# Optimization experiments

Hardware: AMD Instinct MI355X
Metric: run time of the kernel (lower is better)

The kernel has to match this reference:

```python
import jax, jax.numpy as jnp
import numpy as np

BSZ, IN_DIM, OUT_DIM = 512, 1024, 2048
M_AND = 5        # Anderson memory (self.m)
BETA = 1.0
LAM = 1e-4
ALPHA = 1.0
TOL = 1e-5
MAX_ITER = 50
M_MON = 1.0      # monotonicity parameter of MONSingleFc


def _multiply(A, B, z):
    # MONSingleFc.multiply: (1-m)z - z A^T A + z B^T - z B
    Az = z @ A.T
    return (1.0 - M_MON) * z - Az @ A + z @ B.T - z @ B


def _relu(z):
    return jnp.maximum(z, 0.0)


def _single_it(A, B, z, bias):
    zn = _multiply(A, B, z)
    zn = (1.0 - ALPHA) * z + ALPHA * (zn + bias)
    zn = _relu(zn)
    err = jnp.linalg.norm(zn - z) / (1e-6 + jnp.linalg.norm(zn))
    return zn, err


def _anderson_solve(A, B, bias):
    bsz, d = bias.shape
    dt = bias.dtype
    Z = jnp.zeros((bsz, M_AND, d), dt)
    F = jnp.zeros((bsz, M_AND, d), dt)
    z0 = jnp.zeros((bsz, d), dt)
    f0, _ = _single_it(A, B, z0, bias)
    F = F.at[:, 0].set(f0)
    Z = Z.at[:, 1].set(f0)
    f1, _ = _single_it(A, B, f0, bias)
    F = F.at[:, 1].set(f1)
    eye = jnp.eye(M_AND, dtype=dt)

    def cond(s):
        Z, F, it, err = s
        return (it < MAX_ITER) & (err > TOL)

    def body(s):
        Z, F, it, _ = s
        n = jnp.minimum(M_AND, it)
        mask = jnp.arange(M_AND) < n                         # active Anderson slots
        # For it < m the unused slots of Z and F are still zero, so G = F - Z
        # has zero rows there and GGt's Frobenius norm matches the :n slice.
        G = F - Z                                            # (bsz, m, d)
        GGt = jnp.einsum('bmd,bnd->bmn', G, G)
        nrm = jnp.linalg.norm(GGt.reshape(GGt.shape[0], -1), axis=-1)
        GGt = GGt / (nrm[:, None, None] + 1e-6)
        pair = mask[:, None] & mask[None, :]
        # identity padding on inactive slots keeps the solve well-posed and
        # yields alpha = 0 there, equivalent to slicing [:n+1, :n+1].
        Hb = jnp.where(pair, GGt + LAM * eye, eye)
        mk = mask.astype(dt)
        H = jnp.zeros((bsz, M_AND + 1, M_AND + 1), dt)
        H = H.at[:, 0, 1:].set(mk).at[:, 1:, 0].set(mk).at[:, 1:, 1:].set(Hb)
        y = jnp.zeros((bsz, M_AND + 1, 1), dt).at[:, 0, 0].set(1.0)
        alpha = jnp.linalg.solve(H, y)[:, 1:, 0]             # (bsz, m)
        z_new = BETA * jnp.einsum('bm,bmd->bd', alpha, F) \
              + (1.0 - BETA) * jnp.einsum('bm,bmd->bd', alpha, Z)
        slot = it % M_AND
        Z = Z.at[:, slot].set(z_new)
        zo, err = _single_it(A, B, z_new, bias)
        F = F.at[:, slot].set(zo)
        return Z, F, it + 1, err

    Z, F, it, err = jax.lax.while_loop(
        cond, body, (Z, F, jnp.array(2, jnp.int32), jnp.array(jnp.inf, dt)))
    slot = (it - 1) % M_AND
    return Z[:, slot]


def setup_inputs():
    key = jax.random.key(0)
    kx, ka, kb, kw, kub = jax.random.split(key, 5)
    s = 1.0 / np.sqrt(OUT_DIM).astype(np.float32)
    x = jax.random.normal(kx, (BSZ, IN_DIM), jnp.float32)
    # scaled so ||W|| < 1 -> forward-backward splitting converges (trained MON regime)
    A = 0.3 * s * jax.random.normal(ka, (OUT_DIM, OUT_DIM), jnp.float32)
    B = 0.1 * s * jax.random.normal(kb, (OUT_DIM, OUT_DIM), jnp.float32)
    U_W = (1.0 / np.sqrt(IN_DIM).astype(np.float32)) * jax.random.normal(kw, (OUT_DIM, IN_DIM), jnp.float32)
    U_b = 0.01 * jax.random.normal(kub, (OUT_DIM,), jnp.float32)
    return {"x": x, "A": A, "B": B, "U_W": U_W, "U_b": U_b}


def reference(x, A, B, U_W, U_b):
    bias = x @ U_W.T + U_b                       # linear_module.bias(x)
    z_star = _anderson_solve(A, B, bias)         # equilibrium (no-grad in torch)
    zn = _relu(_multiply(A, B, z_star) + bias)   # final full step: nonlin(linear(x, z*))
    return zn
```

## Files before the change

### kernel.cpp

```cpp
#include <hip/hip_runtime.h>
#include <hip/hip_bf16.h>
#include <math.h>

#define BSZ      512
#define IN_DIM   1024
#define OUT_DIM  2048
#define M_AND    5
#define LAM      1e-4f
#define TOL      1e-5f
#define MAX_ITER 50
#define SPLIT_IT 24
#define NBLK     256
#define ITERBLK  512

typedef __bf16 bf16x8 __attribute__((ext_vector_type(8)));
typedef float  f32x4  __attribute__((ext_vector_type(4)));
typedef unsigned short u16x8 __attribute__((ext_vector_type(8)));
typedef unsigned short u16x4 __attribute__((ext_vector_type(4)));
typedef __hip_bfloat16 bf16;

#define GAS __attribute__((address_space(1)))
#define LAS __attribute__((address_space(3)))

#define S_WAITCNT_VMCNT(N) asm volatile("s_waitcnt vmcnt(" #N ")" ::: "memory")

union BU { bf16 b; unsigned short u; };

__device__ __forceinline__ float bf2f(unsigned short u) {
    union { unsigned int i; float f; } c; c.i = (unsigned int)u << 16; return c.f;
}
__device__ __forceinline__ unsigned short f2bf(float f) {
    BU t; t.b = __float2bfloat16(f); return t.u;
}

static constexpr size_t BIAS_B = 0;
static constexpr size_t F_B    = BIAS_B + (size_t)BSZ * OUT_DIM * 4;
static constexpr size_t G_B    = F_B    + (size_t)BSZ * M_AND * OUT_DIM * 4;
static constexpr size_t ZH_B   = G_B    + (size_t)BSZ * M_AND * OUT_DIM * 2;
static constexpr size_t ZL_B   = ZH_B   + (size_t)BSZ * OUT_DIM * 2;
static constexpr size_t XH_B   = ZL_B   + (size_t)BSZ * OUT_DIM * 2;
static constexpr size_t XL_B   = XH_B   + (size_t)BSZ * IN_DIM * 2;
static constexpr size_t UH_B   = XL_B   + (size_t)BSZ * IN_DIM * 2;
static constexpr size_t UL_B   = UH_B   + (size_t)OUT_DIM * IN_DIM * 2;
static constexpr size_t AT_B   = UL_B   + (size_t)OUT_DIM * IN_DIM * 2;
static constexpr size_t WT_B   = AT_B   + (size_t)OUT_DIM * OUT_DIM * 2;
static constexpr size_t RED_B  = WT_B   + (size_t)OUT_DIM * OUT_DIM * 2;
static constexpr size_t BAR_B  = RED_B  + 512;
static constexpr size_t CTR_B  = BAR_B  + 64;
static constexpr size_t FLAG_B = CTR_B  + 256;
static constexpr size_t FSLOT_B = FLAG_B + 16;
static constexpr size_t CTRL_SZ = 512 + 64 + 256 + 16 + 16;

template<int ROUNDS>
__device__ __forceinline__ void stage_tile(const void* __restrict__ g0, int row_bytes,
                                           void* l0, int tid)
{
    #pragma unroll
    for (int q = 0; q < ROUNDS; ++q) {
        const int D   = q * 4096 + tid * 16;
        const int r   = D >> 7;
        const int cb  = D & 127;
        const int scb = cb ^ ((r & 7) << 4);
        const char* gsrc = (const char*)g0 + (size_t)r * row_bytes + scb;
        char* ldst = (char*)l0 + q * 4096 + (tid >> 6) * 1024;
        __builtin_amdgcn_global_load_lds((const GAS void*)gsrc, (LAS void*)ldst, 16, 0, 0);
    }
}

__device__ __forceinline__ bf16x8 read_frag(const void* tile, int row, int cb)
{
    return *(const bf16x8*)((const char*)tile + row * 128 + (cb ^ ((row & 7) << 4)));
}

__device__ __forceinline__ void gsync(unsigned int* bar)
{
    __syncthreads();
    if (threadIdx.x == 0) {
        __threadfence();
        const unsigned int g =
            __hip_atomic_load(&bar[1], __ATOMIC_ACQUIRE, __HIP_MEMORY_SCOPE_AGENT);
        const unsigned int a =
            __hip_atomic_fetch_add(&bar[0], 1u, __ATOMIC_ACQ_REL, __HIP_MEMORY_SCOPE_AGENT);
        if (a == NBLK - 1) {
            __hip_atomic_store(&bar[0], 0u, __ATOMIC_RELAXED, __HIP_MEMORY_SCOPE_AGENT);
            __hip_atomic_fetch_add(&bar[1], 1u, __ATOMIC_RELEASE, __HIP_MEMORY_SCOPE_AGENT);
        } else {
            while (__hip_atomic_load(&bar[1], __ATOMIC_ACQUIRE, __HIP_MEMORY_SCOPE_AGENT) == g)
                __builtin_amdgcn_s_sleep(1);
        }
        __threadfence();
    }
    __syncthreads();
}

__global__ __launch_bounds__(256)
void conv_hilo(const float* __restrict__ src, bf16* __restrict__ h, bf16* __restrict__ l)
{
    const size_t i4 = ((size_t)blockIdx.x * 256 + threadIdx.x) * 4;
    const float4 v = *(const float4*)&src[i4];
    const float vv[4] = {v.x, v.y, v.z, v.w};
    union { short4 s4; unsigned short u[4]; } ph, pl;
    #pragma unroll
    for (int j = 0; j < 4; ++j) {
        ph.u[j] = f2bf(vv[j]);
        pl.u[j] = f2bf(vv[j] - bf2f(ph.u[j]));
    }
    *(short4*)((char*)h + i4 * 2) = ph.s4;
    *(short4*)((char*)l + i4 * 2) = pl.s4;
}

__global__ __launch_bounds__(256)
void prep_at(const float* __restrict__ A, bf16* __restrict__ At)
{
    __shared__ float t[64][65];
    const int tid = threadIdx.x;
    const int k0 = blockIdx.y * 64, c0 = blockIdx.x * 64;
    const int cc = tid & 63, rr = tid >> 6;
    #pragma unroll
    for (int q = 0; q < 16; ++q)
        t[rr + 4 * q][cc] = A[(size_t)(k0 + rr + 4 * q) * OUT_DIM + c0 + cc];
    __syncthreads();
    #pragma unroll
    for (int q = 0; q < 16; ++q)
        At[(size_t)(c0 + rr + 4 * q) * OUT_DIM + k0 + cc] = __float2bfloat16(t[cc][rr + 4 * q]);
}

__global__ __launch_bounds__(256)
void w_mfma(const bf16* __restrict__ At, const float* __restrict__ Bm, bf16* __restrict__ Wt)
{
    __shared__ __align__(16) bf16 lds[2][2][64 * 64];
    const int tid = threadIdx.x;
    const int lane = tid & 63, wid = tid >> 6;
    const int wy = wid >> 1, wx = wid & 1;

    int bb = blockIdx.x;
    int ti = (int)((sqrtf(8.f * bb + 1.f) - 1.f) * 0.5f);
    while ((ti + 1) * (ti + 2) / 2 <= bb) ++ti;
    while (ti * (ti + 1) / 2 > bb) --ti;
    const int tj = bb - ti * (ti + 1) / 2;
    const int r0 = ti * 64, c0 = tj * 64;
    const bool diag = (ti == tj);

    f32x4 acc[2][2];
    #pragma unroll
    for (int i = 0; i < 2; ++i)
        #pragma unroll
        for (int j = 0; j < 2; ++j) acc[i][j] = 0;

    stage_tile<2>(At + (size_t)r0 * OUT_DIM, OUT_DIM * 2, lds[0][0], tid);
    stage_tile<2>(At + (size_t)c0 * OUT_DIM, OUT_DIM * 2, lds[0][1], tid);
    __syncthreads();
    int cur = 0;
    for (int t = 0; t < 32; ++t) {
        if (t + 1 < 32) {
            const int kk = (t + 1) * 64;
            stage_tile<2>(At + (size_t)r0 * OUT_DIM + kk, OUT_DIM * 2, lds[cur ^ 1][0], tid);
            stage_tile<2>(At + (size_t)c0 * OUT_DIM + kk, OUT_DIM * 2, lds[cur ^ 1][1], tid);
        }
        const bf16* Ta = lds[cur][0];
        const bf16* Tb = lds[cur][1];
        #pragma unroll
        for (int kf = 0; kf < 2; ++kf) {
            const int cb = kf * 64 + (lane >> 4) * 16;
            bf16x8 bfr[2];
            #pragma unroll
            for (int nj = 0; nj < 2; ++nj)
                bfr[nj] = read_frag(Tb, wx * 32 + nj * 16 + (lane & 15), cb);
            #pragma unroll
            for (int mi = 0; mi < 2; ++mi) {
                bf16x8 afr = read_frag(Ta, wy * 32 + mi * 16 + (lane & 15), cb);
                #pragma unroll
                for (int nj = 0; nj < 2; ++nj)
                    acc[mi][nj] = __builtin_amdgcn_mfma_f32_16x16x32_bf16(afr, bfr[nj], acc[mi][nj], 0, 0, 0);
            }
        }
        __syncthreads();
        cur ^= 1;
    }

    #pragma unroll
    for (int mi = 0; mi < 2; ++mi) {
        const int rb = r0 + wy * 32 + mi * 16 + (lane >> 4) * 4;
        #pragma unroll
        for (int nj = 0; nj < 2; ++nj) {
            const int c = c0 + wx * 32 + nj * 16 + (lane & 15);
            const float4 bc = *(const float4*)&Bm[(size_t)c * OUT_DIM + rb];
            const float bcv[4] = {bc.x, bc.y, bc.z, bc.w};
            union { short4 s4; unsigned short u[4]; } p;
            #pragma unroll
            for (int g = 0; g < 4; ++g) {
                const float a = acc[mi][nj][g];
                const float brc = Bm[(size_t)(rb + g) * OUT_DIM + c];
                const float w = bcv[g] - brc - a;
                p.u[g] = f2bf(w);
                if (!diag) {
                    const float wm = brc - bcv[g] - a;
                    *((unsigned short*)Wt + (size_t)(rb + g) * OUT_DIM + c) = f2bf(wm);
                }
            }
            *(short4*)((char*)Wt + ((size_t)c * OUT_DIM + rb) * 2) = p.s4;
        }
    }
}

__global__ __launch_bounds__(256)
void bias_mfma(const bf16* __restrict__ xh, const bf16* __restrict__ xl,
               const bf16* __restrict__ uh, const bf16* __restrict__ ul,
               const float* __restrict__ Ub, float* __restrict__ bias,
               float* __restrict__ F, unsigned short* __restrict__ G,
               unsigned short* __restrict__ zh, unsigned short* __restrict__ zl)
{
    __shared__ __align__(16) bf16 lds[2][4][64 * 64];
    const int tid = threadIdx.x;
    const int lane = tid & 63, wid = tid >> 6;
    const int wy = wid >> 1, wx = wid & 1;
    const int m0 = blockIdx.y * 64, n0 = blockIdx.x * 64;

    f32x4 acc[2][2];
    #pragma unroll
    for (int i = 0; i < 2; ++i)
        #pragma unroll
        for (int j = 0; j < 2; ++j) acc[i][j] = 0;

    stage_tile<2>(xh + (size_t)m0 * IN_DIM, IN_DIM * 2, lds[0][0], tid);
    stage_tile<2>(xl + (size_t)m0 * IN_DIM, IN_DIM * 2, lds[0][1], tid);
    stage_tile<2>(uh + (size_t)n0 * IN_DIM, IN_DIM * 2, lds[0][2], tid);
    stage_tile<2>(ul + (size_t)n0 * IN_DIM, IN_DIM * 2, lds[0][3], tid);
    __syncthreads();
    int cur = 0;
    for (int t = 0; t < 16; ++t) {
        if (t + 1 < 16) {
            const int kk = (t + 1) * 64;
            stage_tile<2>(xh + (size_t)m0 * IN_DIM + kk, IN_DIM * 2, lds[cur ^ 1][0], tid);
            stage_tile<2>(xl + (size_t)m0 * IN_DIM + kk, IN_DIM * 2, lds[cur ^ 1][1], tid);
            stage_tile<2>(uh + (size_t)n0 * IN_DIM + kk, IN_DIM * 2, lds[cur ^ 1][2], tid);
            stage_tile<2>(ul + (size_t)n0 * IN_DIM + kk, IN_DIM * 2, lds[cur ^ 1][3], tid);
        }
        const bf16* Txh = lds[cur][0];
        const bf16* Txl = lds[cur][1];
        const bf16* Tuh = lds[cur][2];
        const bf16* Tul = lds[cur][3];
        #pragma unroll
        for (int kf = 0; kf < 2; ++kf) {
            const int cb = kf * 64 + (lane >> 4) * 16;
            bf16x8 bh[2], bl[2];
            #pragma unroll
            for (int nj = 0; nj < 2; ++nj) {
                const int br = wx * 32 + nj * 16 + (lane & 15);
                bh[nj] = read_frag(Tuh, br, cb);
                bl[nj] = read_frag(Tul, br, cb);
            }
            #pragma unroll
            for (int mi = 0; mi < 2; ++mi) {
                const int ar = wy * 32 + mi * 16 + (lane & 15);
                bf16x8 ah = read_frag(Txh, ar, cb);
                bf16x8 al = read_frag(Txl, ar, cb);
                #pragma unroll
                for (int nj = 0; nj < 2; ++nj) {
                    acc[mi][nj] = __builtin_amdgcn_mfma_f32_16x16x32_bf16(ah, bh[nj], acc[mi][nj], 0, 0, 0);
                    acc[mi][nj] = __builtin_amdgcn_mfma_f32_16x16x32_bf16(ah, bl[nj], acc[mi][nj], 0, 0, 0);
                    acc[mi][nj] = __builtin_amdgcn_mfma_f32_16x16x32_bf16(al, bh[nj], acc[mi][nj], 0, 0, 0);
                }
            }
        }
        __syncthreads();
        cur ^= 1;
    }

    #pragma unroll
    for (int mi = 0; mi < 2; ++mi) {
        const int mb = m0 + wy * 32 + mi * 16 + (lane >> 4) * 4;
        #pragma unroll
        for (int nj = 0; nj < 2; ++nj) {
            const int n = n0 + wx * 32 + nj * 16 + (lane & 15);
            const float ub = Ub[n];
            #pragma unroll
            for (int g = 0; g < 4; ++g) {
                const int m = mb + g;
                const size_t idx = (size_t)m * OUT_DIM + n;
                const float v = acc[mi][nj][g] + ub;
                bias[idx] = v;
                const float f = fmaxf(v, 0.f);
                F[((size_t)m * M_AND + 0) * OUT_DIM + n] = f;
                G[((size_t)m * M_AND + 0) * OUT_DIM + n] = f2bf(f);
                const unsigned short h = f2bf(f);
                zh[idx] = h;
                zl[idx] = f2bf(f - bf2f(h));
            }
        }
    }
}

template<bool DO_ERR>
__device__ __forceinline__ void iter_core(
    const int m0, const int n0, const int tid,
    const unsigned short* __restrict__ zh, const unsigned short* __restrict__ zl,
    const bf16* __restrict__ Wt, const float* __restrict__ bias,
    float* __restrict__ F, unsigned short* __restrict__ G,
    float* red, bf16* lds_buf, const int slot, const int it)
{
    const int lane = tid & 63, wid = tid >> 6;
    const int wy = wid >> 1, wx = wid & 1;
    #define BUFP(s) (lds_buf + (s) * 8192)

    f32x4 acc[2];
    acc[0] = 0; acc[1] = 0;

    auto STAGE = [&](int s, int kk) {
        stage_tile<1>(zh + (size_t)m0 * OUT_DIM + kk, OUT_DIM * 2, BUFP(s), tid);
        stage_tile<1>(zl + (size_t)m0 * OUT_DIM + kk, OUT_DIM * 2, BUFP(s) + 2048, tid);
        stage_tile<2>(Wt + (size_t)n0 * OUT_DIM + kk, OUT_DIM * 2, BUFP(s) + 4096, tid);
    };

    STAGE(0, 0);
    STAGE(1, 64);
    for (int t = 0; t < 32; ++t) {
        const int s = t % 3;
        if (t + 2 < 32) { S_WAITCNT_VMCNT(4); } else { S_WAITCNT_VMCNT(0); }
        __builtin_amdgcn_s_barrier();
        if (t + 2 < 32) STAGE((t + 2) % 3, (t + 2) * 64);
        const bf16* Th = BUFP(s);
        const bf16* Tl = BUFP(s) + 2048;
        const bf16* Tw = BUFP(s) + 4096;
        __builtin_amdgcn_s_setprio(1);
        #pragma unroll
        for (int kf = 0; kf < 2; ++kf) {
            const int cb = kf * 64 + (lane >> 4) * 16;
            bf16x8 b0 = read_frag(Tw, wx * 32 + (lane & 15), cb);
            bf16x8 b1 = read_frag(Tw, wx * 32 + 16 + (lane & 15), cb);
            bf16x8 ah = read_frag(Th, wy * 16 + (lane & 15), cb);
            bf16x8 al = read_frag(Tl, wy * 16 + (lane & 15), cb);
            acc[0] = __builtin_amdgcn_mfma_f32_16x16x32_bf16(ah, b0, acc[0], 0, 0, 0);
            acc[0] = __builtin_amdgcn_mfma_f32_16x16x32_bf16(al, b0, acc[0], 0, 0, 0);
            acc[1] = __builtin_amdgcn_mfma_f32_16x16x32_bf16(ah, b1, acc[1], 0, 0, 0);
            acc[1] = __builtin_amdgcn_mfma_f32_16x16x32_bf16(al, b1, acc[1], 0, 0, 0);
        }
        __builtin_amdgcn_s_setprio(0);
    }
    #undef BUFP

    float lnum = 0.f, lden = 0.f;
    const int mb = m0 + wy * 16 + (lane >> 4) * 4;
    #pragma unroll
    for (int nj = 0; nj < 2; ++nj) {
        const int n = n0 + wx * 32 + nj * 16 + (lane & 15);
        #pragma unroll
        for (int g = 0; g < 4; ++g) {
            const int m = mb + g;
            const size_t idx = (size_t)m * OUT_DIM + n;
            float v = acc[nj][g] + bias[idx];
            v = fmaxf(v, 0.f);
            const float zc = bf2f(zh[idx]) + bf2f(zl[idx]);
            const float gg = v - zc;
            F[((size_t)m * M_AND + slot) * OUT_DIM + n] = v;
            G[((size_t)m * M_AND + slot) * OUT_DIM + n] = f2bf(gg);
            if (DO_ERR) { lnum += gg * gg; lden += v * v; }
        }
    }

    if (DO_ERR) {
        #pragma unroll
        for (int off = 32; off; off >>= 1) {
            lnum += __shfl_down(lnum, off);
            lden += __shfl_down(lden, off);
        }
        __shared__ float swn[4], swd[4];
        if ((tid & 63) == 0) { swn[tid >> 6] = lnum; swd[tid >> 6] = lden; }
        __syncthreads();
        if (tid == 0) {
            atomicAdd(&red[2 * it],     swn[0] + swn[1] + swn[2] + swn[3]);
            atomicAdd(&red[2 * it + 1], swd[0] + swd[1] + swd[2] + swd[3]);
        }
    }
}

__device__ __forceinline__ void swz_mn(int bid, int& m0, int& n0)
{
    const int xcd = bid & 7, sl = bid >> 3;
    n0 = (xcd * 4 + (sl & 3)) * 64;
    m0 = (sl >> 2) * 32;
}

template<bool DO_ERR>
__global__ __launch_bounds__(256)
void iter_mfma(const unsigned short* __restrict__ zh, const unsigned short* __restrict__ zl,
               const bf16* __restrict__ Wt, const float* __restrict__ bias,
               float* __restrict__ F, unsigned short* __restrict__ G,
               float* red, unsigned int* ctr, int* flag, int* fslot, int slot, int it)
{
    if (((volatile int*)flag)[0]) return;
    __shared__ __align__(16) bf16 lds_buf[3 * 8192];
    int m0, n0;
    swz_mn(blockIdx.x, m0, n0);
    iter_core<DO_ERR>(m0, n0, threadIdx.x, zh, zl, Wt, bias, F, G, red, lds_buf, slot, it);
    if (DO_ERR && threadIdx.x == 0) {
        __threadfence();
        const unsigned int done = atomicAdd(&ctr[it], 1u);
        if (done == ITERBLK - 1) {
            ((volatile int*)fslot)[0] = slot;
            const float num2 = ((volatile float*)red)[2 * it];
            const float den2 = ((volatile float*)red)[2 * it + 1];
            if (sqrtf(num2) <= TOL * (1e-6f + sqrtf(den2)))
                ((volatile int*)flag)[0] = 1;
        }
    }
}

__global__ __launch_bounds__(256)
void final_copy(const float* __restrict__ F, const int* __restrict__ fslot,
                float* __restrict__ out)
{
    const int s = ((volatile const int*)fslot)[0];
    const size_t i4 = ((size_t)blockIdx.x * 256 + threadIdx.x) * 4;
    const int m = (int)(i4 >> 11), n = (int)(i4 & 2047);
    *(float4*)&out[i4] = *(const float4*)&F[((size_t)m * M_AND + s) * OUT_DIM + n];
}

__global__ __launch_bounds__(512)
void anderson_kernel(const float* __restrict__ F, const unsigned short* __restrict__ G,
                     unsigned short* __restrict__ zh, unsigned short* __restrict__ zl,
                     int* flag, int it)
{
    if (((volatile int*)flag)[0]) return;
    const int b = blockIdx.x;
    const int tid = threadIdx.x;
    const int lane = tid & 63, wid = tid >> 6;
    const int n = (it < M_AND) ? it : M_AND;
    const int c0 = tid * 4;
    const unsigned short* Gb = G + (size_t)b * M_AND * OUT_DIM;
    const float* Fb = F + (size_t)b * M_AND * OUT_DIM;

    float g[M_AND][4];
    float4 f[M_AND];
    #pragma unroll
    for (int m = 0; m < M_AND; ++m) {
        f[m] = *(const float4*)(Fb + (size_t)m * OUT_DIM + c0);
        if (m < n) {
            const u16x4 gv = *(const u16x4*)(Gb + (size_t)m * OUT_DIM + c0);
            #pragma unroll
            for (int q = 0; q < 4; ++q) g[m][q] = bf2f(gv[q]);
        } else {
            #pragma unroll
            for (int q = 0; q < 4; ++q) g[m][q] = 0.f;
        }
    }

    float dots[15];
    {
        int p = 0;
        #pragma unroll
        for (int i = 0; i < M_AND; ++i)
            #pragma unroll
            for (int j = i; j < M_AND; ++j) {
                float s = 0.f;
                #pragma unroll
                for (int q = 0; q < 4; ++q) s += g[i][q] * g[j][q];
                dots[p++] = s;
            }
    }

    __shared__ float sred[15][8];
    #pragma unroll
    for (int p = 0; p < 15; ++p) {
        float v = dots[p];
        #pragma unroll
        for (int off = 32; off; off >>= 1) v += __shfl_xor(v, off);
        if (lane == 0) sred[p][wid] = v;
    }
    __syncthreads();

    __shared__ float s_alpha[M_AND];
    if (tid == 0) {
        float GGm[M_AND][M_AND];
        int p = 0;
        for (int i = 0; i < M_AND; ++i)
            for (int j = i; j < M_AND; ++j) {
                float v = 0.f;
                for (int w = 0; w < 8; ++w) v += sred[p][w];
                GGm[i][j] = v; GGm[j][i] = v; ++p;
            }
        float fro = 0.f;
        for (int i = 0; i < M_AND; ++i)
            for (int j = 0; j < M_AND; ++j) fro += GGm[i][j] * GGm[i][j];
        const float inv = 1.f / (sqrtf(fro) + 1e-6f);

        float Mm[M_AND][M_AND];
        for (int i = 0; i < n; ++i)
            for (int j = 0; j < n; ++j)
                Mm[i][j] = GGm[i][j] * inv + (i == j ? LAM : 0.f);

        float L[M_AND][M_AND];
        for (int i = 0; i < n; ++i)
            for (int j = 0; j <= i; ++j) {
                float s = Mm[i][j];
                for (int k = 0; k < j; ++k) s -= L[i][k] * L[j][k];
                L[i][j] = (i == j) ? sqrtf(fmaxf(s, 1e-20f)) : s / L[j][j];
            }
        float y[M_AND], u[M_AND];
        for (int i = 0; i < n; ++i) {
            float s = 1.f;
            for (int k = 0; k < i; ++k) s -= L[i][k] * y[k];
            y[i] = s / L[i][i];
        }
        for (int i = n - 1; i >= 0; --i) {
            float s = y[i];
            for (int k = i + 1; k < n; ++k) s -= L[k][i] * u[k];
            u[i] = s / L[i][i];
        }
        float su = 0.f;
        for (int i = 0; i < n; ++i) su += u[i];
        const float isu = 1.f / su;
        for (int m = 0; m < M_AND; ++m) s_alpha[m] = (m < n) ? u[m] * isu : 0.f;
    }
    __syncthreads();

    float z[4] = {};
    #pragma unroll
    for (int m = 0; m < M_AND; ++m) {
        if (m < n) {
            const float a = s_alpha[m];
            z[0] += a * f[m].x; z[1] += a * f[m].y;
            z[2] += a * f[m].z; z[3] += a * f[m].w;
        }
    }
    u16x4 hv, lv;
    #pragma unroll
    for (int q = 0; q < 4; ++q) {
        const unsigned short h = f2bf(z[q]);
        hv[q] = h;
        lv[q] = f2bf(z[q] - bf2f(h));
    }
    *(u16x4*)(zh + (size_t)b * OUT_DIM + c0) = hv;
    *(u16x4*)(zl + (size_t)b * OUT_DIM + c0) = lv;
}

__global__ __launch_bounds__(256)
void tail_loop(unsigned short* zh, unsigned short* zl,
               const bf16* __restrict__ Wt, const float* __restrict__ bias,
               float* F, unsigned short* G,
               float* red, unsigned int* bar, int* flag, int* fslot)
{
    if (((volatile int*)flag)[0]) return;
    __shared__ __align__(16) bf16 lds_buf[3 * 8192];
    __shared__ float sred2[2][2][15];
    __shared__ float s_alpha[2][M_AND];
    const int bid = blockIdx.x, tid = threadIdx.x;
    int m0a, n0a, m0b, n0b;
    swz_mn(bid, m0a, n0a);
    swz_mn(bid + 256, m0b, n0b);

    for (int it = SPLIT_IT; it < MAX_ITER; ++it) {
        {
            const int half = tid >> 7, lt = tid & 127;
            const int r = bid * 2 + half;
            const int wv = lt >> 6;
            const unsigned short* Gb = G + (size_t)r * M_AND * OUT_DIM;
            const float* Fb = F + (size_t)r * M_AND * OUT_DIM;
            const int c0 = lt * 16;

            float g[M_AND][16];
            #pragma unroll
            for (int m = 0; m < M_AND; ++m) {
                const u16x8 ga = *(const u16x8*)(Gb + (size_t)m * OUT_DIM + c0);
                const u16x8 gb2 = *(const u16x8*)(Gb + (size_t)m * OUT_DIM + c0 + 8);
                #pragma unroll
                for (int q = 0; q < 8; ++q) { g[m][q] = bf2f(ga[q]); g[m][8 + q] = bf2f(gb2[q]); }
            }
            {
                int p = 0;
                #pragma unroll
                for (int i = 0; i < M_AND; ++i)
                    #pragma unroll
                    for (int j = i; j < M_AND; ++j) {
                        float s = 0.f;
                        #pragma unroll
                        for (int q = 0; q < 16; ++q) s += g[i][q] * g[j][q];
                        float v = s;
                        #pragma unroll
                        for (int off = 32; off; off >>= 1) v += __shfl_xor(v, off);
                        if ((lt & 63) == 0) sred2[half][wv][p] = v;
                        ++p;
                    }
            }
            __syncthreads();
            if (lt == 0) {
                float GGm[M_AND][M_AND];
                int p = 0;
                for (int i = 0; i < M_AND; ++i)
                    for (int j = i; j < M_AND; ++j) {
                        const float v = sred2[half][0][p] + sred2[half][1][p];
                        GGm[i][j] = v; GGm[j][i] = v; ++p;
                    }
                float fro = 0.f;
                for (int i = 0; i < M_AND; ++i)
                    for (int j = 0; j < M_AND; ++j) fro += GGm[i][j] * GGm[i][j];
                const float inv = 1.f / (sqrtf(fro) + 1e-6f);
                float Mm[M_AND][M_AND];
                for (int i = 0; i < M_AND; ++i)
                    for (int j = 0; j < M_AND; ++j)
                        Mm[i][j] = GGm[i][j] * inv + (i == j ? LAM : 0.f);
                float L[M_AND][M_AND];
                for (int i = 0; i < M_AND; ++i)
                    for (int j = 0; j <= i; ++j) {
                        float s = Mm[i][j];
                        for (int k = 0; k < j; ++k) s -= L[i][k] * L[j][k];
                        L[i][j] = (i == j) ? sqrtf(fmaxf(s, 1e-20f)) : s / L[j][j];
                    }
                float y[M_AND], u[M_AND];
                for (int i = 0; i < M_AND; ++i) {
                    float s = 1.f;
                    for (int k = 0; k < i; ++k) s -= L[i][k] * y[k];
                    y[i] = s / L[i][i];
                }
                for (int i = M_AND - 1; i >= 0; --i) {
                    float s = y[i];
                    for (int k = i + 1; k < M_AND; ++k) s -= L[k][i] * u[k];
                    u[i] = s / L[i][i];
                }
                float su = 0.f;
                for (int i = 0; i < M_AND; ++i) su += u[i];
                const float isu = 1.f / su;
                for (int m = 0; m < M_AND; ++m) s_alpha[half][m] = u[m] * isu;
            }
            __syncthreads();
            float z[16] = {};
            for (int m = 0; m < M_AND; ++m) {
                const float a = s_alpha[half][m];
                #pragma unroll
                for (int q = 0; q < 4; ++q) {
                    const float4 fv = *(const float4*)(Fb + (size_t)m * OUT_DIM + c0 + q * 4);
                    z[q * 4 + 0] += a * fv.x; z[q * 4 + 1] += a * fv.y;
                    z[q * 4 + 2] += a * fv.z; z[q * 4 + 3] += a * fv.w;
                }
            }
            u16x8 hv[2], lv[2];
            #pragma unroll
            for (int q = 0; q < 16; ++q) {
                const unsigned short h = f2bf(z[q]);
                hv[q >> 3][q & 7] = h;
                lv[q >> 3][q & 7] = f2bf(z[q] - bf2f(h));
            }
            const size_t base = (size_t)r * OUT_DIM + c0;
            *(u16x8*)(zh + base)     = hv[0];
            *(u16x8*)(zh + base + 8) = hv[1];
            *(u16x8*)(zl + base)     = lv[0];
            *(u16x8*)(zl + base + 8) = lv[1];
        }
        gsync(bar);
        iter_core<true>(m0a, n0a, tid, zh, zl, Wt, bias, F, G, red, lds_buf, it % M_AND, it);
        iter_core<true>(m0b, n0b, tid, zh, zl, Wt, bias, F, G, red, lds_buf, it % M_AND, it);
        gsync(bar);
        if (bid == 0 && tid == 0) ((volatile int*)fslot)[0] = it % M_AND;
        const float num2 = __hip_atomic_load(&red[2 * it], __ATOMIC_RELAXED, __HIP_MEMORY_SCOPE_AGENT);
        const float den2 = __hip_atomic_load(&red[2 * it + 1], __ATOMIC_RELAXED, __HIP_MEMORY_SCOPE_AGENT);
        if (sqrtf(num2) <= TOL * (1e-6f + sqrtf(den2))) break;
    }
}

extern "C" void kernel_launch(void* const* d_in, const int* in_sizes, int n_in,
                              void* d_out, int out_size, void* d_ws, size_t ws_size,
                              hipStream_t stream)
{
    const float* x  = (const float*)d_in[0];
    const float* A  = (const float*)d_in[1];
    const float* B  = (const float*)d_in[2];
    const float* UW = (const float*)d_in[3];
    const float* Ub = (const float*)d_in[4];
    float* out = (float*)d_out;
    char*  wsb = (char*)d_ws;

    float*          bias = (float*)(wsb + BIAS_B);
    float*          F    = (float*)(wsb + F_B);
    unsigned short* G    = (unsigned short*)(wsb + G_B);
    unsigned short* zh   = (unsigned short*)(wsb + ZH_B);
    unsigned short* zl   = (unsigned short*)(wsb + ZL_B);
    bf16*           xh   = (bf16*)(wsb + XH_B);
    bf16*           xl   = (bf16*)(wsb + XL_B);
    bf16*           uh   = (bf16*)(wsb + UH_B);
    bf16*           ul   = (bf16*)(wsb + UL_B);
    bf16*           At   = (bf16*)(wsb + AT_B);
    bf16*           Wt   = (bf16*)(wsb + WT_B);
    float*          red  = (float*)(wsb + RED_B);
    unsigned int*   bar  = (unsigned int*)(wsb + BAR_B);
    unsigned int*   ctr  = (unsigned int*)(wsb + CTR_B);
    int*            flag = (int*)(wsb + FLAG_B);
    int*            fslot= (int*)(wsb + FSLOT_B);

    hipMemsetAsync(wsb + RED_B, 0, CTRL_SZ, stream);

    conv_hilo<<<dim3(BSZ * IN_DIM / 1024),     256, 0, stream>>>(x,  xh, xl);
    conv_hilo<<<dim3(OUT_DIM * IN_DIM / 1024), 256, 0, stream>>>(UW, uh, ul);
    prep_at  <<<dim3(32, 32), 256, 0, stream>>>(A, At);
    w_mfma   <<<dim3(528), 256, 0, stream>>>(At, B, Wt);
    bias_mfma<<<dim3(32, 8), 256, 0, stream>>>(xh, xl, uh, ul, Ub, bias, F, G, zh, zl);

    iter_mfma<false><<<dim3(ITERBLK), 256, 0, stream>>>(zh, zl, Wt, bias, F, G,
                                                        red, ctr, flag, fslot, 1, 0);

    for (int it = 2; it < SPLIT_IT; ++it) {
        anderson_kernel<<<dim3(BSZ), 512, 0, stream>>>(F, G, zh, zl, flag, it);
        iter_mfma<true><<<dim3(ITERBLK), 256, 0, stream>>>(zh, zl, Wt, bias, F, G,
                                                           red, ctr, flag, fslot, it % M_AND, it);
    }
    tail_loop<<<dim3(NBLK), 256, 0, stream>>>(zh, zl, Wt, bias, F, G, red, bar, flag, fslot);
    final_copy<<<dim3(BSZ * OUT_DIM / 1024), 256, 0, stream>>>(F, fslot, out);
}
```

Baseline: 602.2 us.

## Replace async LDS staging with register-prefetched double buffer in iteration GEMM

The iteration GEMM core now prefetches the global z-hi, z-lo and weight tiles two steps ahead into registers, then writes them into a swizzled two-stage LDS double buffer, instead of using the three-stage direct-to-LDS staging. This shrinks LDS per block so that two blocks can reside per CU, which the iteration kernel now requests through a launch-bounds hint. It adds an extra barrier and register pressure in each step, plus a __syncthreads between the two tiles in the persistent tail loop so the reused buffer is not overwritten early. The switch to the persistent tail loop also moves earlier, from iteration 24 to iteration 16.

```diff
diff --git a/kernel.cpp b/kernel.cpp
--- a/kernel.cpp
+++ b/kernel.cpp
@@ -9,7 +9,7 @@
 #define LAM      1e-4f
 #define TOL      1e-5f
 #define MAX_ITER 50
-#define SPLIT_IT 24
+#define SPLIT_IT 16
 #define NBLK     256
 #define ITERBLK  512
 
@@ -301,43 +301,73 @@
 {
     const int lane = tid & 63, wid = tid >> 6;
     const int wy = wid >> 1, wx = wid & 1;
-    #define BUFP(s) (lds_buf + (s) * 8192)
+
+    const int Dz  = tid * 16;
+    const int zr  = Dz >> 7,  zcb  = Dz & 127;
+    const size_t z_ro = (size_t)zr * 4096 + zcb;
+    const int zo_l = zr * 128 + (zcb ^ ((zr & 7) << 4));
+    const int Dw1 = 4096 + tid * 16;
+    const int wr0 = Dz >> 7,  wcb0 = Dz & 127;
+    const int wr1 = Dw1 >> 7, wcb1 = Dw1 & 127;
+    const size_t w_ro0 = (size_t)wr0 * 4096 + wcb0;
+    const size_t w_ro1 = (size_t)wr1 * 4096 + wcb1;
+    const int wo_l0 = wr0 * 128 + (wcb0 ^ ((wr0 & 7) << 4));
+    const int wo_l1 = wr1 * 128 + (wcb1 ^ ((wr1 & 7) << 4));
+
+    const char* zbase = (const char*)zh + (size_t)m0 * 4096;
+    const char* lbase = (const char*)zl + (size_t)m0 * 4096;
+    const char* wbase = (const char*)Wt + (size_t)n0 * 4096;
 
     f32x4 acc[2];
     acc[0] = 0; acc[1] = 0;
 
-    auto STAGE = [&](int s, int kk) {
-        stage_tile<1>(zh + (size_t)m0 * OUT_DIM + kk, OUT_DIM * 2, BUFP(s), tid);
-        stage_tile<1>(zl + (size_t)m0 * OUT_DIM + kk, OUT_DIM * 2, BUFP(s) + 2048, tid);
-        stage_tile<2>(Wt + (size_t)n0 * OUT_DIM + kk, OUT_DIM * 2, BUFP(s) + 4096, tid);
-    };
-
-    STAGE(0, 0);
-    STAGE(1, 64);
-    for (int t = 0; t < 32; ++t) {
-        const int s = t % 3;
-        if (t + 2 < 32) { S_WAITCNT_VMCNT(4); } else { S_WAITCNT_VMCNT(0); }
-        __builtin_amdgcn_s_barrier();
-        if (t + 2 < 32) STAGE((t + 2) % 3, (t + 2) * 64);
-        const bf16* Th = BUFP(s);
-        const bf16* Tl = BUFP(s) + 2048;
-        const bf16* Tw = BUFP(s) + 4096;
-        __builtin_amdgcn_s_setprio(1);
-        #pragma unroll
-        for (int kf = 0; kf < 2; ++kf) {
-            const int cb = kf * 64 + (lane >> 4) * 16;
-            bf16x8 b0 = read_frag(Tw, wx * 32 + (lane & 15), cb);
-            bf16x8 b1 = read_frag(Tw, wx * 32 + 16 + (lane & 15), cb);
-            bf16x8 ah = read_frag(Th, wy * 16 + (lane & 15), cb);
-            bf16x8 al = read_frag(Tl, wy * 16 + (lane & 15), cb);
-            acc[0] = __builtin_amdgcn_mfma_f32_16x16x32_bf16(ah, b0, acc[0], 0, 0, 0);
-            acc[0] = __builtin_amdgcn_mfma_f32_16x16x32_bf16(al, b0, acc[0], 0, 0, 0);
-            acc[1] = __builtin_amdgcn_mfma_f32_16x16x32_bf16(ah, b1, acc[1], 0, 0, 0);
-            acc[1] = __builtin_amdgcn_mfma_f32_16x16x32_bf16(al, b1, acc[1], 0, 0, 0);
-        }
-        __builtin_amdgcn_s_setprio(0);
-    }
-    #undef BUFP
+    float4 rza, rla, rw0a, rw1a, rzb, rlb, rw0b, rw1b;
+
+#define LOADR_(RZ, RL, RW0, RW1, KK)                                         \
+    RZ  = *(const float4*)(zbase + (size_t)(KK) * 2 + z_ro);                 \
+    RL  = *(const float4*)(lbase + (size_t)(KK) * 2 + z_ro);                 \
+    RW0 = *(const float4*)(wbase + (size_t)(KK) * 2 + w_ro0);                \
+    RW1 = *(const float4*)(wbase + (size_t)(KK) * 2 + w_ro1);
+
+#define STEP_(T, RZ, RL, RW0, RW1, CUR)                                      \
+  {                                                                          \
+    if ((T) + 1 < 32) { S_WAITCNT_VMCNT(4); } else { S_WAITCNT_VMCNT(0); }   \
+    __builtin_amdgcn_s_barrier();          \
+    char* bp = (char*)lds_buf + (CUR) * 16384;                               \
+    *(float4*)(bp + zo_l)         = RZ;                                      \
+    *(float4*)(bp + 4096 + zo_l)  = RL;                                      \
+    *(float4*)(bp + 8192 + wo_l0) = RW0;                                     \
+    *(float4*)(bp + 8192 + wo_l1) = RW1;                                     \
+    if ((T) + 2 < 32) { LOADR_(RZ, RL, RW0, RW1, ((T) + 2) * 64); }          \
+    asm volatile("s_waitcnt lgkmcnt(0)" ::: "memory");                       \
+    __builtin_amdgcn_sched_barrier(0);                                       \
+    __builtin_amdgcn_s_barrier();         \
+    __builtin_amdgcn_sched_barrier(0);                                       \
+    __builtin_amdgcn_s_setprio(1);                                           \
+    _Pragma("unroll")                                                        \
+    for (int kf = 0; kf < 2; ++kf) {                                         \
+        const int cb2 = kf * 64 + (lane >> 4) * 16;                          \
+        bf16x8 b0  = read_frag(bp + 8192, wx * 32 + (lane & 15), cb2);       \
+        bf16x8 b1  = read_frag(bp + 8192, wx * 32 + 16 + (lane & 15), cb2);  \
+        bf16x8 ahv = read_frag(bp,        wy * 16 + (lane & 15), cb2);       \
+        bf16x8 alv = read_frag(bp + 4096, wy * 16 + (lane & 15), cb2);       \
+        acc[0] = __builtin_amdgcn_mfma_f32_16x16x32_bf16(ahv, b0, acc[0], 0, 0, 0); \
+        acc[0] = __builtin_amdgcn_mfma_f32_16x16x32_bf16(alv, b0, acc[0], 0, 0, 0); \
+        acc[1] = __builtin_amdgcn_mfma_f32_16x16x32_bf16(ahv, b1, acc[1], 0, 0, 0); \
+        acc[1] = __builtin_amdgcn_mfma_f32_16x16x32_bf16(alv, b1, acc[1], 0, 0, 0); \
+    }                                                                        \
+    __builtin_amdgcn_s_setprio(0);                                           \
+  }
+
+    LOADR_(rza, rla, rw0a, rw1a, 0);
+    LOADR_(rzb, rlb, rw0b, rw1b, 64);
+    for (int tb = 0; tb < 16; ++tb) {
+        const int t0 = 2 * tb;
+        STEP_(t0,     rza, rla, rw0a, rw1a, 0);
+        STEP_(t0 + 1, rzb, rlb, rw0b, rw1b, 1);
+    }
+#undef STEP_
+#undef LOADR_
 
     float lnum = 0.f, lden = 0.f;
     const int mb = m0 + wy * 16 + (lane >> 4) * 4;
@@ -382,14 +412,14 @@
 }
 
 template<bool DO_ERR>
-__global__ __launch_bounds__(256)
+__global__ __launch_bounds__(256, 2)
 void iter_mfma(const unsigned short* __restrict__ zh, const unsigned short* __restrict__ zl,
                const bf16* __restrict__ Wt, const float* __restrict__ bias,
                float* __restrict__ F, unsigned short* __restrict__ G,
                float* red, unsigned int* ctr, int* flag, int* fslot, int slot, int it)
 {
     if (((volatile int*)flag)[0]) return;
-    __shared__ __align__(16) bf16 lds_buf[3 * 8192];
+    __shared__ __align__(16) bf16 lds_buf[2 * 8192];
     int m0, n0;
     swz_mn(blockIdx.x, m0, n0);
     iter_core<DO_ERR>(m0, n0, threadIdx.x, zh, zl, Wt, bias, F, G, red, lds_buf, slot, it);
@@ -541,7 +571,7 @@
                float* red, unsigned int* bar, int* flag, int* fslot)
 {
     if (((volatile int*)flag)[0]) return;
-    __shared__ __align__(16) bf16 lds_buf[3 * 8192];
+    __shared__ __align__(16) bf16 lds_buf[2 * 8192];
     __shared__ float sred2[2][2][15];
     __shared__ float s_alpha[2][M_AND];
     const int bid = blockIdx.x, tid = threadIdx.x;
@@ -648,6 +678,7 @@
         }
         gsync(bar);
         iter_core<true>(m0a, n0a, tid, zh, zl, Wt, bias, F, G, red, lds_buf, it % M_AND, it);
+        __syncthreads();
         iter_core<true>(m0b, n0b, tid, zh, zl, Wt, bias, F, G, red, lds_buf, it % M_AND, it);
         gsync(bar);
         if (bid == 0 && tid == 0) ((volatile int*)fslot)[0] = it % M_AND;
```

New measurement: 527.5 us. 12.4% less time.
